# Kernel optimization log

Hardware: AMD Instinct MI355X
Metric: run time of the kernel (lower is better)

Reference implementation:

```python
import jax, jax.numpy as jnp
import numpy as np

N = 100_000   # total vertices
E = 1_600_000 # total directed edges
B = 64        # graphs in batch
HID = 128
DM = 256
EPS = 1e-5


def _linear_init(k, fan_in, fan_out):
    lim = 1.0 / np.sqrt(fan_in)
    kw, kb = jax.random.split(k)
    W = jax.random.uniform(kw, (fan_in, fan_out), minval=-lim, maxval=lim, dtype=jnp.float32)
    b = jax.random.uniform(kb, (fan_out,), minval=-lim, maxval=lim, dtype=jnp.float32)
    return W, b


def setup_inputs() -> dict:
    key = jax.random.key(0)
    ks = jax.random.split(key, 8)
    W_in, b_in = _linear_init(ks[0], 3, HID)
    W1, b1 = _linear_init(ks[1], HID, HID)
    W2, b2 = _linear_init(ks[2], HID, HID)
    W3, b3 = _linear_init(ks[3], HID, HID)
    W_out, b_out = _linear_init(ks[4], HID, DM)
    vertices = jax.random.normal(ks[5], (N, 3), dtype=jnp.float32)
    edge_index = jax.random.randint(ks[6], (2, E), 0, N)
    batch = jnp.sort(jax.random.randint(ks[7], (N,), 0, B))
    gamma = jnp.ones((DM,), jnp.float32)
    beta = jnp.zeros((DM,), jnp.float32)
    return dict(vertices=vertices, edge_index=edge_index, batch=batch,
                W_in=W_in, b_in=b_in, W1=W1, b1=b1, W2=W2, b2=b2, W3=W3, b3=b3,
                W_out=W_out, b_out=b_out, gamma=gamma, beta=beta)


def _gcn_conv(x, W, b, src, dst):
    # PyG GCNConv: add self-loops, sym-normalize by deg^{-1/2}, aggregate at dst.
    h = x @ W  # [N, HID]
    deg = jnp.zeros((x.shape[0],), x.dtype).at[dst].add(1.0) + 1.0  # +1 self-loop
    dinv = jax.lax.rsqrt(deg)
    msg = h[src] * (dinv[src] * dinv[dst])[:, None]       # [E, HID] gather+scale
    agg = jnp.zeros_like(h).at[dst].add(msg)               # scatter-add
    agg = agg + h * (dinv * dinv)[:, None]                 # self-loop contribution
    return agg + b


def reference(vertices, edge_index, batch, W_in, b_in, W1, b1, W2, b2, W3, b3, W_out, b_out, gamma, beta):
    src, dst = edge_index[0], edge_index[1]
    x = vertices @ W_in + b_in
    for W, b in ((W1, b1), (W2, b2), (W3, b3)):
        x = jax.nn.relu(_gcn_conv(x, W, b, src, dst))
    # global_mean_pool over batch segments
    summ = jax.ops.segment_sum(x, batch, num_segments=B)
    cnt = jax.ops.segment_sum(jnp.ones((x.shape[0], 1), x.dtype), batch, num_segments=B)
    pooled = summ / jnp.maximum(cnt, 1.0)
    y = pooled @ W_out + b_out
    mu = jnp.mean(y, axis=-1, keepdims=True)
    var = jnp.var(y, axis=-1, keepdims=True)
    return (y - mu) * jax.lax.rsqrt(var + EPS) * gamma + beta
```

## Files before the change

### kernel.cpp

```cpp
#include <hip/hip_runtime.h>

constexpr int NV = 100000;
constexpr int NE = 1600000;
constexpr int NB = 64;
constexpr int HD = 128;
constexpr int DM = 256;
#define EPSLN 1e-5f

constexpr int DPB   = 512;
constexpr int NBUCK = (NV + DPB - 1) / DPB;
constexpr int BCAP  = 16384;
constexpr int EPB   = 4096;
constexpr int NEB   = (NE + EPB - 1) / EPB;

typedef short bf16x8 __attribute__((ext_vector_type(8)));
typedef float f32x4 __attribute__((ext_vector_type(4)));

__device__ inline unsigned short f2b(float f) {
    union { float f; unsigned u; } x; x.f = f;
    unsigned r = x.u + 0x7FFF + ((x.u >> 16) & 1);
    return (unsigned short)(r >> 16);
}
__device__ inline float b2f(unsigned short h) {
    union { unsigned u; float f; } x; x.u = (unsigned)h << 16;
    return x.f;
}

__global__ __launch_bounds__(256) void k_bscatter(const int* __restrict__ ei,
                                                  int* __restrict__ bcursor,
                                                  int* __restrict__ ebuf) {
    __shared__ int h[NBUCK];
    __shared__ int lbase[NBUCK];
    int t = threadIdx.x;
    for (int i = t; i < NBUCK; i += 256) h[i] = 0;
    __syncthreads();
    int base = blockIdx.x * EPB;
    int s[16], d[16], rk[16];
    #pragma unroll
    for (int j = 0; j < 16; ++j) {
        int idx = base + j * 256 + t;
        if (idx < NE) {
            s[j] = ei[idx];
            d[j] = ei[NE + idx];
            rk[j] = atomicAdd(&h[d[j] >> 9], 1);
        } else d[j] = -1;
    }
    __syncthreads();
    for (int i = t; i < NBUCK; i += 256) {
        int c = h[i];
        if (c) lbase[i] = atomicAdd(&bcursor[i], c);
    }
    __syncthreads();
    #pragma unroll
    for (int j = 0; j < 16; ++j)
        if (d[j] >= 0) {
            int b = d[j] >> 9;
            ebuf[(b << 14) + lbase[b] + rk[j]] = (s[j] << 9) | (d[j] & 511);
        }
}

__global__ __launch_bounds__(256) void k_bcsr(const int* __restrict__ ebuf,
                                              const int* __restrict__ bcursor,
                                              int* __restrict__ degi,
                                              float* __restrict__ dinv,
                                              int* __restrict__ rowstart,
                                              int* __restrict__ csr) {
    __shared__ int h[DPB];
    __shared__ int sdata[256];
    int b = blockIdx.x, t = threadIdx.x, d0 = b * DPB;
    for (int i = t; i < DPB; i += 256) h[i] = 0;
    __syncthreads();
    int e0 = b << 14;
    int e1 = e0 + bcursor[b];
    for (int e = e0 + t; e < e1; e += 256) atomicAdd(&h[ebuf[e] & 511], 1);
    __syncthreads();
    int a = h[2 * t], c = h[2 * t + 1];
    sdata[t] = a + c;
    __syncthreads();
    for (int off = 1; off < 256; off <<= 1) {
        int v = sdata[t];
        int add = (t >= off) ? sdata[t - off] : 0;
        __syncthreads();
        sdata[t] = v + add;
        __syncthreads();
    }
    int excl = (t == 0) ? 0 : sdata[t - 1];
    int base = e0;
    int v0 = d0 + 2 * t, v1 = v0 + 1;
    if (v0 < NV) { rowstart[v0] = base + excl;     degi[v0] = a; dinv[v0] = rsqrtf((float)a + 1.0f); }
    if (v1 < NV) { rowstart[v1] = base + excl + a; degi[v1] = c; dinv[v1] = rsqrtf((float)c + 1.0f); }
    h[2 * t]     = base + excl;
    h[2 * t + 1] = base + excl + a;
    __syncthreads();
    for (int e = e0 + t; e < e1; e += 256) {
        int p = ebuf[e];
        int slot = atomicAdd(&h[p & 511], 1);
        csr[slot] = p >> 9;
    }
}

__global__ __launch_bounds__(256) void k_h1(const float* __restrict__ verts,
                                            const float* __restrict__ Win,
                                            const float* __restrict__ bin,
                                            const float* __restrict__ W1,
                                            unsigned short* __restrict__ Hb) {
    __shared__ float Wc[3 * HD];
    __shared__ float bc[HD];
    int t = threadIdx.x;
    if (t < HD) {
        float w0 = 0.f, w1 = 0.f, w2 = 0.f, bv = 0.f;
        for (int k = 0; k < HD; ++k) {
            float w = W1[k * HD + t];
            w0 = fmaf(Win[k], w, w0);
            w1 = fmaf(Win[128 + k], w, w1);
            w2 = fmaf(Win[256 + k], w, w2);
            bv = fmaf(bin[k], w, bv);
        }
        Wc[t] = w0; Wc[128 + t] = w1; Wc[256 + t] = w2; bc[t] = bv;
    }
    __syncthreads();
    for (int idx = blockIdx.x * 256 + t; idx < NV * HD; idx += gridDim.x * 256) {
        int v = idx >> 7, c = idx & 127;
        float a = verts[v * 3 + 0], b = verts[v * 3 + 1], d = verts[v * 3 + 2];
        Hb[idx] = f2b(bc[c] + a * Wc[c] + b * Wc[128 + c] + d * Wc[256 + c]);
    }
}

__global__ void k_wt2(const float* __restrict__ W2, const float* __restrict__ W3,
                      unsigned short* __restrict__ Wt) {
    int idx = blockIdx.x * 256 + threadIdx.x;
    if (idx >= 2 * HD * HD) return;
    int l = idx >> 14, r = idx & 16383;
    const float* W = (l == 0) ? W2 : W3;
    int n = r >> 7, k = r & 127;
    Wt[idx - r + n * HD + k] = f2b(W[k * HD + n]);
}

__global__ __launch_bounds__(256) void k_gemm_mfma(const unsigned short* __restrict__ Xb,
                                                   const unsigned short* __restrict__ Wt,
                                                   unsigned short* __restrict__ Hb) {
    __shared__ __align__(16) unsigned short hs[4][16][136];
    int wave = threadIdx.x >> 6;
    int lane = threadIdx.x & 63;
    int r = lane & 15;
    int g = lane >> 4;
    int row0 = blockIdx.x * 64 + wave * 16;
    int arow = row0 + r;
    bool valid = arow < NV;

    bf16x8 afrag[4];
    const unsigned short* xp = Xb + (size_t)arow * HD + g * 8;
    #pragma unroll
    for (int ks = 0; ks < 4; ++ks) {
        if (valid) afrag[ks] = *(const bf16x8*)(xp + ks * 32);
        else       afrag[ks] = bf16x8{0, 0, 0, 0, 0, 0, 0, 0};
    }

    #pragma unroll
    for (int nt = 0; nt < 8; ++nt) {
        f32x4 acc = {0.f, 0.f, 0.f, 0.f};
        const unsigned short* wp = Wt + (size_t)(nt * 16 + r) * HD + g * 8;
        #pragma unroll
        for (int ks = 0; ks < 4; ++ks) {
            bf16x8 bfrag = *(const bf16x8*)(wp + ks * 32);
            acc = __builtin_amdgcn_mfma_f32_16x16x32_bf16(afrag[ks], bfrag, acc, 0, 0, 0);
        }
        #pragma unroll
        for (int j = 0; j < 4; ++j)
            hs[wave][g * 4 + j][nt * 16 + r] = f2b(acc[j]);
    }
    __syncthreads();
    int row = lane >> 2;
    int grow = row0 - wave * 16 + (threadIdx.x >> 2 & 0xFFFF);
    grow = blockIdx.x * 64 + wave * 16 + row;
    #pragma unroll
    for (int k = 0; k < 4; ++k) {
        int c = (lane & 3) + k * 4;
        bf16x8 val = *(const bf16x8*)&hs[wave][row][c * 8];
        if (grow < NV)
            *(bf16x8*)(Hb + (size_t)grow * HD + c * 8) = val;
    }
}

__global__ __launch_bounds__(256) void k_agg(const unsigned short* __restrict__ H,
                                             const float* __restrict__ dinv,
                                             const int* __restrict__ rowstart,
                                             const int* __restrict__ degi,
                                             const int* __restrict__ csr_src,
                                             const float* __restrict__ bias,
                                             unsigned short* __restrict__ Xo) {
    int gtid = blockIdx.x * 256 + threadIdx.x;
    int v = gtid >> 6;
    if (v >= NV) return;
    int lane = threadIdx.x & 63;
    int q = lane >> 4;
    int l4 = lane & 15;
    float di = dinv[v];
    int rs = rowstart[v], len = degi[v];
    float a[8];
    if (q == 0) {
        float sc = di * di;
        bf16x8 hv = *(const bf16x8*)(H + (size_t)v * HD + l4 * 8);
        #pragma unroll
        for (int jj = 0; jj < 8; ++jj) a[jj] = b2f((unsigned short)hv[jj]) * sc;
    } else {
        #pragma unroll
        for (int jj = 0; jj < 8; ++jj) a[jj] = 0.f;
    }
    int cnt = (len - q + 3) >> 2;
    int idx = rs + q;
    int j = 0;
    for (; j + 1 < cnt; j += 2) {
        int s0 = csr_src[idx], s1 = csr_src[idx + 4];
        idx += 8;
        float w0 = dinv[s0] * di, w1 = dinv[s1] * di;
        bf16x8 h0 = *(const bf16x8*)(H + (size_t)s0 * HD + l4 * 8);
        bf16x8 h1 = *(const bf16x8*)(H + (size_t)s1 * HD + l4 * 8);
        #pragma unroll
        for (int jj = 0; jj < 8; ++jj) {
            a[jj] = fmaf(b2f((unsigned short)h0[jj]), w0, a[jj]);
            a[jj] = fmaf(b2f((unsigned short)h1[jj]), w1, a[jj]);
        }
    }
    if (j < cnt) {
        int s0 = csr_src[idx];
        float w0 = dinv[s0] * di;
        bf16x8 h0 = *(const bf16x8*)(H + (size_t)s0 * HD + l4 * 8);
        #pragma unroll
        for (int jj = 0; jj < 8; ++jj)
            a[jj] = fmaf(b2f((unsigned short)h0[jj]), w0, a[jj]);
    }
    #pragma unroll
    for (int jj = 0; jj < 8; ++jj) {
        a[jj] += __shfl_xor(a[jj], 16);
        a[jj] += __shfl_xor(a[jj], 32);
    }
    if (q == 0) {
        bf16x8 ov;
        #pragma unroll
        for (int jj = 0; jj < 8; ++jj)
            ov[jj] = (short)f2b(fmaxf(a[jj] + bias[l4 * 8 + jj], 0.f));
        *(bf16x8*)(Xo + (size_t)v * HD + l4 * 8) = ov;
    }
}

__global__ __launch_bounds__(256) void k_pool(const unsigned short* __restrict__ X,
                                              const int* __restrict__ batch,
                                              float* __restrict__ pool,
                                              int* __restrict__ cnt) {
    constexpr int NCHUNK = 2048;
    constexpr int CHUNK = (NV + NCHUNK - 1) / NCHUNK;
    int c = threadIdx.x & 127;
    int r = threadIdx.x >> 7;
    int v0 = blockIdx.x * CHUNK;
    if (v0 >= NV) return;
    int vend = min(v0 + CHUNK, NV);
    int cur = -1;
    float sum = 0.f;
    for (int v = v0 + r; v < vend; v += 2) {
        int bb = batch[v];
        if (bb != cur) {
            if (cur >= 0) atomicAdd(&pool[cur * HD + c], sum);
            cur = bb; sum = 0.f;
        }
        sum += b2f(X[(size_t)v * HD + c]);
    }
    if (cur >= 0) atomicAdd(&pool[cur * HD + c], sum);
    if (threadIdx.x == 0) {
        int prev = batch[v0]; int c0 = 0;
        for (int v = v0; v < vend; ++v) {
            int bb = batch[v];
            if (bb != prev) { atomicAdd(&cnt[prev], c0); prev = bb; c0 = 0; }
            ++c0;
        }
        atomicAdd(&cnt[prev], c0);
    }
}

__global__ __launch_bounds__(256) void k_out(const float* __restrict__ pool,
                                             const int* __restrict__ cnt,
                                             const float* __restrict__ Wout,
                                             const float* __restrict__ bout,
                                             const float* __restrict__ gamma,
                                             const float* __restrict__ beta,
                                             float* __restrict__ out) {
    __shared__ float ps[HD];
    __shared__ float red[DM];
    int g = blockIdx.x, t = threadIdx.x;
    if (t < HD) {
        float cn = fmaxf((float)cnt[g], 1.0f);
        ps[t] = pool[g * HD + t] / cn;
    }
    __syncthreads();
    float acc = bout[t];
    #pragma unroll 8
    for (int k = 0; k < HD; ++k) acc = fmaf(ps[k], Wout[k * DM + t], acc);
    red[t] = acc; __syncthreads();
    for (int s2 = 128; s2 > 0; s2 >>= 1) {
        if (t < s2) red[t] += red[t + s2];
        __syncthreads();
    }
    float mu = red[0] * (1.0f / DM);
    __syncthreads();
    float d = acc - mu;
    red[t] = d * d; __syncthreads();
    for (int s2 = 128; s2 > 0; s2 >>= 1) {
        if (t < s2) red[t] += red[t + s2];
        __syncthreads();
    }
    float var = red[0] * (1.0f / DM);
    out[g * DM + t] = d * rsqrtf(var + EPSLN) * gamma[t] + beta[t];
}

extern "C" void kernel_launch(void* const* d_in, const int* in_sizes, int n_in,
                              void* d_out, int out_size, void* d_ws, size_t ws_size,
                              hipStream_t stream) {
    const float* verts = (const float*)d_in[0];
    const int*   ei    = (const int*)d_in[1];
    const int*   batch = (const int*)d_in[2];
    const float* Win   = (const float*)d_in[3];
    const float* bin   = (const float*)d_in[4];
    const float* W1    = (const float*)d_in[5];
    const float* b1    = (const float*)d_in[6];
    const float* W2    = (const float*)d_in[7];
    const float* b2    = (const float*)d_in[8];
    const float* W3    = (const float*)d_in[9];
    const float* b3    = (const float*)d_in[10];
    const float* Wout  = (const float*)d_in[11];
    const float* bout  = (const float*)d_in[12];
    const float* gamma = (const float*)d_in[13];
    const float* beta  = (const float*)d_in[14];
    float* out = (float*)d_out;

    char* wp = (char*)d_ws;
    auto alloc = [&](size_t bytes) -> char* {
        char* p = wp;
        wp += (bytes + 255) & ~(size_t)255;
        return p;
    };
    unsigned short* bufA = (unsigned short*)alloc((size_t)NV * HD * 2);
    unsigned short* bufB = (unsigned short*)alloc((size_t)NV * HD * 2);
    unsigned short* Wt   = (unsigned short*)alloc((size_t)2 * HD * HD * 2);
    int*   degi     = (int*)alloc((size_t)NV * 4);
    float* dinv     = (float*)alloc((size_t)NV * 4);
    int*   rowstart = (int*)alloc((size_t)NV * 4);
    int*   csr      = (int*)alloc((size_t)NBUCK * BCAP * 4);
    int*   ebuf     = (int*)alloc((size_t)NBUCK * BCAP * 4);
    int*   bcursor  = (int*)alloc((size_t)NBUCK * 4);
    float* pool     = (float*)alloc((size_t)NB * HD * 4);
    int*   cnt      = (int*)alloc((size_t)NB * 4);

    hipMemsetAsync(bcursor, 0, (size_t)NBUCK * 4, stream);
    hipMemsetAsync(pool,    0, (size_t)NB * HD * 4, stream);
    hipMemsetAsync(cnt,     0, (size_t)NB * 4, stream);

    k_bscatter<<<NEB, 256, 0, stream>>>(ei, bcursor, ebuf);
    k_bcsr<<<NBUCK, 256, 0, stream>>>(ebuf, bcursor, degi, dinv, rowstart, csr);

    k_wt2<<<(2 * HD * HD + 255) / 256, 256, 0, stream>>>(W2, W3, Wt);
    k_h1<<<1024, 256, 0, stream>>>(verts, Win, bin, W1, bufA);

    int aggrid = (int)(((size_t)NV * 64 + 255) / 256);
    k_agg<<<aggrid, 256, 0, stream>>>(bufA, dinv, rowstart, degi, csr, b1, bufB);
    k_gemm_mfma<<<(NV + 63) / 64, 256, 0, stream>>>(bufB, Wt, bufA);
    k_agg<<<aggrid, 256, 0, stream>>>(bufA, dinv, rowstart, degi, csr, b2, bufB);
    k_gemm_mfma<<<(NV + 63) / 64, 256, 0, stream>>>(bufB, Wt + (size_t)HD * HD, bufA);
    k_agg<<<aggrid, 256, 0, stream>>>(bufA, dinv, rowstart, degi, csr, b3, bufB);

    k_pool<<<2048, 256, 0, stream>>>(bufB, batch, pool, cnt);
    k_out<<<NB, 256, 0, stream>>>(pool, cnt, Wout, bout, gamma, beta, out);
}
```

Measured before the change: 375.5 us.

## Merge prep kernels, stage GEMM weights in LDS, vectorize pooling, coalesce memsets

Merges the weight-transpose kernel into the first-layer projection kernel and combines three memsets into one, cutting launch and host overhead. The MFMA GEMM now copies the 128x128 bf16 weight matrix into padded shared memory once per block instead of reading B fragments from global memory. Pooling reads 8 bf16 values per load and, when a chunk spans at most two graphs, reduces in shared memory before doing global atomics. Each GEMM block now pays to load the full weight matrix into LDS, and the shared-memory footprint grows.

```diff
diff --git a/kernel.cpp b/kernel.cpp
--- a/kernel.cpp
+++ b/kernel.cpp
@@ -99,14 +99,27 @@
     }
 }
 
-__global__ __launch_bounds__(256) void k_h1(const float* __restrict__ verts,
-                                            const float* __restrict__ Win,
-                                            const float* __restrict__ bin,
-                                            const float* __restrict__ W1,
-                                            unsigned short* __restrict__ Hb) {
+__global__ __launch_bounds__(256) void k_prep(const float* __restrict__ verts,
+                                              const float* __restrict__ Win,
+                                              const float* __restrict__ bin,
+                                              const float* __restrict__ W1,
+                                              const float* __restrict__ W2,
+                                              const float* __restrict__ W3,
+                                              unsigned short* __restrict__ Hb,
+                                              unsigned short* __restrict__ Wt) {
+    int t = threadIdx.x;
+    if (blockIdx.x >= 1024) {
+        int idx = (blockIdx.x - 1024) * 256 + t;
+        if (idx < 2 * HD * HD) {
+            int l = idx >> 14, r = idx & 16383;
+            const float* W = (l == 0) ? W2 : W3;
+            int n = r >> 7, k = r & 127;
+            Wt[(l << 14) + n * HD + k] = f2b(W[k * HD + n]);
+        }
+        return;
+    }
     __shared__ float Wc[3 * HD];
     __shared__ float bc[HD];
-    int t = threadIdx.x;
     if (t < HD) {
         float w0 = 0.f, w1 = 0.f, w2 = 0.f, bv = 0.f;
         for (int k = 0; k < HD; ++k) {
@@ -119,29 +132,30 @@
         Wc[t] = w0; Wc[128 + t] = w1; Wc[256 + t] = w2; bc[t] = bv;
     }
     __syncthreads();
-    for (int idx = blockIdx.x * 256 + t; idx < NV * HD; idx += gridDim.x * 256) {
+    for (int idx = blockIdx.x * 256 + t; idx < NV * HD; idx += 1024 * 256) {
         int v = idx >> 7, c = idx & 127;
         float a = verts[v * 3 + 0], b = verts[v * 3 + 1], d = verts[v * 3 + 2];
         Hb[idx] = f2b(bc[c] + a * Wc[c] + b * Wc[128 + c] + d * Wc[256 + c]);
     }
 }
 
-__global__ void k_wt2(const float* __restrict__ W2, const float* __restrict__ W3,
-                      unsigned short* __restrict__ Wt) {
-    int idx = blockIdx.x * 256 + threadIdx.x;
-    if (idx >= 2 * HD * HD) return;
-    int l = idx >> 14, r = idx & 16383;
-    const float* W = (l == 0) ? W2 : W3;
-    int n = r >> 7, k = r & 127;
-    Wt[idx - r + n * HD + k] = f2b(W[k * HD + n]);
-}
-
 __global__ __launch_bounds__(256) void k_gemm_mfma(const unsigned short* __restrict__ Xb,
                                                    const unsigned short* __restrict__ Wt,
                                                    unsigned short* __restrict__ Hb) {
+    __shared__ __align__(16) unsigned short Ws[128 * 132];
     __shared__ __align__(16) unsigned short hs[4][16][136];
-    int wave = threadIdx.x >> 6;
-    int lane = threadIdx.x & 63;
+    int t = threadIdx.x;
+    {
+        int row = t >> 1;
+        int half = (t & 1) << 6;
+        const unsigned short* src = Wt + row * HD + half;
+        unsigned short* dst = &Ws[row * 132 + half];
+        #pragma unroll
+        for (int i = 0; i < 8; ++i)
+            *(bf16x8*)(dst + i * 8) = *(const bf16x8*)(src + i * 8);
+    }
+    int wave = t >> 6;
+    int lane = t & 63;
     int r = lane & 15;
     int g = lane >> 4;
     int row0 = blockIdx.x * 64 + wave * 16;
@@ -155,24 +169,22 @@
         if (valid) afrag[ks] = *(const bf16x8*)(xp + ks * 32);
         else       afrag[ks] = bf16x8{0, 0, 0, 0, 0, 0, 0, 0};
     }
+    __syncthreads();
 
     #pragma unroll
     for (int nt = 0; nt < 8; ++nt) {
         f32x4 acc = {0.f, 0.f, 0.f, 0.f};
-        const unsigned short* wp = Wt + (size_t)(nt * 16 + r) * HD + g * 8;
         #pragma unroll
         for (int ks = 0; ks < 4; ++ks) {
-            bf16x8 bfrag = *(const bf16x8*)(wp + ks * 32);
+            bf16x8 bfrag = *(const bf16x8*)&Ws[(nt * 16 + r) * 132 + g * 8 + ks * 32];
             acc = __builtin_amdgcn_mfma_f32_16x16x32_bf16(afrag[ks], bfrag, acc, 0, 0, 0);
         }
         #pragma unroll
         for (int j = 0; j < 4; ++j)
             hs[wave][g * 4 + j][nt * 16 + r] = f2b(acc[j]);
     }
-    __syncthreads();
     int row = lane >> 2;
-    int grow = row0 - wave * 16 + (threadIdx.x >> 2 & 0xFFFF);
-    grow = blockIdx.x * 64 + wave * 16 + row;
+    int grow = row0 + row;
     #pragma unroll
     for (int k = 0; k < 4; ++k) {
         int c = (lane & 3) + k * 4;
@@ -248,26 +260,67 @@
                                               const int* __restrict__ batch,
                                               float* __restrict__ pool,
                                               int* __restrict__ cnt) {
-    constexpr int NCHUNK = 2048;
-    constexpr int CHUNK = (NV + NCHUNK - 1) / NCHUNK;
-    int c = threadIdx.x & 127;
-    int r = threadIdx.x >> 7;
+    constexpr int CHUNK = (NV + 2047) / 2048;
+    __shared__ float lp[2][HD];
+    __shared__ int binfo[2];
+    int t = threadIdx.x;
     int v0 = blockIdx.x * CHUNK;
     if (v0 >= NV) return;
     int vend = min(v0 + CHUNK, NV);
-    int cur = -1;
-    float sum = 0.f;
-    for (int v = v0 + r; v < vend; v += 2) {
-        int bb = batch[v];
-        if (bb != cur) {
-            if (cur >= 0) atomicAdd(&pool[cur * HD + c], sum);
-            cur = bb; sum = 0.f;
-        }
-        sum += b2f(X[(size_t)v * HD + c]);
-    }
-    if (cur >= 0) atomicAdd(&pool[cur * HD + c], sum);
-    if (threadIdx.x == 0) {
-        int prev = batch[v0]; int c0 = 0;
+    if (t < 2 * HD) ((float*)lp)[t] = 0.f;
+    if (t == 0) { binfo[0] = batch[v0]; binfo[1] = batch[vend - 1]; }
+    __syncthreads();
+    int b0 = binfo[0], b1 = binfo[1];
+    int cg = t & 15;
+    int ro = t >> 4;
+    if (b1 - b0 <= 1) {
+        float a0[8] = {}, a1[8] = {};
+        for (int v = v0 + ro; v < vend; v += 16) {
+            bf16x8 x = *(const bf16x8*)(X + (size_t)v * HD + cg * 8);
+            if (batch[v] == b0) {
+                #pragma unroll
+                for (int jj = 0; jj < 8; ++jj) a0[jj] += b2f((unsigned short)x[jj]);
+            } else {
+                #pragma unroll
+                for (int jj = 0; jj < 8; ++jj) a1[jj] += b2f((unsigned short)x[jj]);
+            }
+        }
+        #pragma unroll
+        for (int jj = 0; jj < 8; ++jj) {
+            atomicAdd(&lp[0][cg * 8 + jj], a0[jj]);
+            if (b1 != b0) atomicAdd(&lp[1][cg * 8 + jj], a1[jj]);
+        }
+        __syncthreads();
+        int slot = t >> 7, col = t & 127;
+        if (slot == 0 || b1 != b0)
+            atomicAdd(&pool[(slot ? b1 : b0) * HD + col], lp[slot][col]);
+    } else {
+        float a[8] = {};
+        int cur = -1;
+        for (int v = v0 + ro; v < vend; v += 16) {
+            int bb = batch[v];
+            if (bb != cur) {
+                if (cur >= 0) {
+                    #pragma unroll
+                    for (int jj = 0; jj < 8; ++jj) {
+                        atomicAdd(&pool[cur * HD + cg * 8 + jj], a[jj]);
+                        a[jj] = 0.f;
+                    }
+                }
+                cur = bb;
+            }
+            bf16x8 x = *(const bf16x8*)(X + (size_t)v * HD + cg * 8);
+            #pragma unroll
+            for (int jj = 0; jj < 8; ++jj) a[jj] += b2f((unsigned short)x[jj]);
+        }
+        if (cur >= 0) {
+            #pragma unroll
+            for (int jj = 0; jj < 8; ++jj)
+                atomicAdd(&pool[cur * HD + cg * 8 + jj], a[jj]);
+        }
+    }
+    if (t == 0) {
+        int prev = batch[v0], c0 = 0;
         for (int v = v0; v < vend; ++v) {
             int bb = batch[v];
             if (bb != prev) { atomicAdd(&cnt[prev], c0); prev = bb; c0 = 0; }
@@ -346,19 +399,17 @@
     int*   rowstart = (int*)alloc((size_t)NV * 4);
     int*   csr      = (int*)alloc((size_t)NBUCK * BCAP * 4);
     int*   ebuf     = (int*)alloc((size_t)NBUCK * BCAP * 4);
-    int*   bcursor  = (int*)alloc((size_t)NBUCK * 4);
-    float* pool     = (float*)alloc((size_t)NB * HD * 4);
-    int*   cnt      = (int*)alloc((size_t)NB * 4);
-
-    hipMemsetAsync(bcursor, 0, (size_t)NBUCK * 4, stream);
-    hipMemsetAsync(pool,    0, (size_t)NB * HD * 4, stream);
-    hipMemsetAsync(cnt,     0, (size_t)NB * 4, stream);
+    char*  zblock   = alloc(1024 + (size_t)NB * HD * 4 + 1024);
+    int*   bcursor  = (int*)zblock;
+    float* pool     = (float*)(zblock + 1024);
+    int*   cnt      = (int*)(zblock + 1024 + (size_t)NB * HD * 4);
+
+    hipMemsetAsync(zblock, 0, 1024 + (size_t)NB * HD * 4 + 1024, stream);
 
     k_bscatter<<<NEB, 256, 0, stream>>>(ei, bcursor, ebuf);
     k_bcsr<<<NBUCK, 256, 0, stream>>>(ebuf, bcursor, degi, dinv, rowstart, csr);
 
-    k_wt2<<<(2 * HD * HD + 255) / 256, 256, 0, stream>>>(W2, W3, Wt);
-    k_h1<<<1024, 256, 0, stream>>>(verts, Win, bin, W1, bufA);
+    k_prep<<<1152, 256, 0, stream>>>(verts, Win, bin, W1, W2, W3, bufA, Wt);
 
     int aggrid = (int)(((size_t)NV * 64 + 255) / 256);
     k_agg<<<aggrid, 256, 0, stream>>>(bufA, dinv, rowstart, degi, csr, b1, bufB);
```

Measured after the change: 345.5 us. -8.0%, faster.
